# Kernel optimization log

Hardware: AMD Instinct MI355X
Metric: run time of the kernel (lower is better)

Reference implementation:

```python
import jax, jax.numpy as jnp
import numpy as np

B, T, C, H = 2, 2048, 1024, 16


def setup_inputs() -> dict:
    key = jax.random.key(0)
    ks = jax.random.split(key, 9)
    s = 1.0 / np.sqrt(C)
    return {
        "query": jax.random.normal(ks[0], (B, T, C), dtype=jnp.float32),
        "Wq": jax.random.normal(ks[1], (C, C), dtype=jnp.float32) * s,
        "bq": jnp.zeros((C,), dtype=jnp.float32),
        "Wk": jax.random.normal(ks[2], (C, C), dtype=jnp.float32) * s,
        "bk": jnp.zeros((C,), dtype=jnp.float32),
        "Wv": jax.random.normal(ks[3], (C, C), dtype=jnp.float32) * s,
        "bv": jnp.zeros((C,), dtype=jnp.float32),
        "Wp": jax.random.normal(ks[4], (C, C), dtype=jnp.float32) * s,
        "bp": jnp.zeros((C,), dtype=jnp.float32),
        "n_head": H,
    }


def reference(query, Wq, bq, Wk, bk, Wv, bv, Wp, bp, n_head):
    b, t, c = query.shape
    d = c // n_head
    # QKV projections -> [b, h, t, d]
    q = (query @ Wq + bq).reshape(b, t, n_head, d).transpose(0, 2, 1, 3)
    k = (query @ Wk + bk).reshape(b, t, n_head, d).transpose(0, 2, 1, 3)
    v = (query @ Wv + bv).reshape(b, t, n_head, d).transpose(0, 2, 1, 3)
    scale = 1.0 / jnp.sqrt(jnp.asarray(d, dtype=query.dtype))
    att = jnp.einsum('bhtd,bhsd->bhts', q, k) * scale  # [b,h,t,t]
    causal = jnp.tril(jnp.ones((t, t), dtype=bool))
    att = jnp.where(causal[None, None, :, :], att, -jnp.inf)
    att = jax.nn.softmax(att, axis=-1)
    y = jnp.einsum('bhts,bhsd->bhtd', att, v)  # [b,h,t,d]
    y = y.transpose(0, 2, 1, 3).reshape(b, t, c)
    return y @ Wp + bp
```

## Files before the change

### kernel.cpp

```cpp
#include <hip/hip_runtime.h>
#include <math.h>

#define B_ 2
#define T_ 2048
#define C_ 1024
#define H_ 16
#define D_ 64
#define M_ (B_*T_)

typedef __bf16 bf16x8 __attribute__((ext_vector_type(8)));
typedef __bf16 bf16x4 __attribute__((ext_vector_type(4)));
typedef float  f32x4  __attribute__((ext_vector_type(4)));
typedef float  f32x16 __attribute__((ext_vector_type(16)));

__device__ __forceinline__ unsigned short f2bf(float f) {
    unsigned int u = __float_as_uint(f);
    u += 0x7FFFu + ((u >> 16) & 1u);
    return (unsigned short)(u >> 16);
}

__device__ __forceinline__ bf16x8 pack4(unsigned a, unsigned b,
                                        unsigned c, unsigned d) {
    union { unsigned u[4]; bf16x8 v; } t;
    t.u[0] = a; t.u[1] = b; t.u[2] = c; t.u[3] = d;
    return t.v;
}

__device__ __forceinline__ void gload16(const void* g, void* l) {
    __builtin_amdgcn_global_load_lds(
        (const __attribute__((address_space(1))) void*)g,
        (__attribute__((address_space(3))) void*)l, 16, 0, 0);
}

__global__ __launch_bounds__(256) void prep_kernel(
    const float* __restrict__ X, unsigned short* __restrict__ Xb,
    const float* __restrict__ W0, const float* __restrict__ W1,
    const float* __restrict__ W2, const float* __restrict__ W3,
    unsigned short* __restrict__ T0, unsigned short* __restrict__ T1,
    unsigned short* __restrict__ T2, unsigned short* __restrict__ T3)
{
    const int tid = threadIdx.x;
    if (blockIdx.x < 2048) {
        const size_t i = ((size_t)blockIdx.x * 256 + tid) * 8;
        const float4 a = *(const float4*)&X[i];
        const float4 b = *(const float4*)&X[i + 4];
        ushort4 s0, s1;
        s0.x = f2bf(a.x); s0.y = f2bf(a.y); s0.z = f2bf(a.z); s0.w = f2bf(a.w);
        s1.x = f2bf(b.x); s1.y = f2bf(b.y); s1.z = f2bf(b.z); s1.w = f2bf(b.w);
        *(ushort4*)&Xb[i]     = s0;
        *(ushort4*)&Xb[i + 4] = s1;
        return;
    }
    const int bz = blockIdx.x - 2048;
    const int z = bz >> 10, rem = bz & 1023;
    const float* W; unsigned short* Wt;
    switch (z) {
        case 0: W = W0; Wt = T0; break;
        case 1: W = W1; Wt = T1; break;
        case 2: W = W2; Wt = T2; break;
        default: W = W3; Wt = T3; break;
    }
    __shared__ unsigned short tile[32][33];
    const int k0 = (rem >> 5) * 32, n0 = (rem & 31) * 32;
    {
        const int r = tid >> 3, c = (tid & 7) * 4;
        const float4 v = *(const float4*)&W[(size_t)(k0 + r)*C_ + n0 + c];
        tile[c+0][r] = f2bf(v.x);
        tile[c+1][r] = f2bf(v.y);
        tile[c+2][r] = f2bf(v.z);
        tile[c+3][r] = f2bf(v.w);
    }
    __syncthreads();
    {
        const int r = tid >> 3, c = (tid & 7) * 4;
        ushort4 s;
        s.x = tile[r][c+0]; s.y = tile[r][c+1]; s.z = tile[r][c+2]; s.w = tile[r][c+3];
        *(ushort4*)&Wt[(size_t)(n0 + r)*C_ + k0 + c] = s;
    }
}

__global__ __launch_bounds__(256) void gemm_proj_kernel(
    const unsigned short* __restrict__ A, const unsigned short* __restrict__ Bt,
    const float* __restrict__ bias, float* __restrict__ out)
{
    __shared__ __align__(16) unsigned short Als[2][64 * 32];
    __shared__ __align__(16) unsigned short Bls[2][128 * 32];

    const int tid  = threadIdx.x;
    const int lane = tid & 63;
    const int wave = tid >> 6;
    const int wm = wave >> 1, wn = wave & 1;
    const int l15 = lane & 15, quad = lane >> 4;
    const int m0 = blockIdx.y * 64, n0 = blockIdx.x * 128;
    const int srow = lane >> 2;
    const int scol = (lane & 3) * 8;

    const f32x4 zero4 = {0.f, 0.f, 0.f, 0.f};
    f32x4 acc[2][4];
    #pragma unroll
    for (int i = 0; i < 2; ++i)
        #pragma unroll
        for (int j = 0; j < 4; ++j) acc[i][j] = zero4;

    for (int k0 = 0; k0 < C_; k0 += 64) {
        __syncthreads();
        #pragma unroll
        for (int h = 0; h < 2; ++h) {
            gload16(&A[(size_t)(m0 + wave*16 + srow)*C_ + k0 + h*32 + scol],
                    &Als[h][(wave*16)*32]);
            #pragma unroll
            for (int u = 0; u < 2; ++u) {
                const int r = wave*32 + u*16 + srow;
                gload16(&Bt[(size_t)(n0 + r)*C_ + k0 + h*32 + scol],
                        &Bls[h][(wave*32 + u*16)*32]);
            }
        }
        __syncthreads();

        #pragma unroll
        for (int h = 0; h < 2; ++h) {
            bf16x8 af[2], bfr[4];
            #pragma unroll
            for (int i = 0; i < 2; ++i)
                af[i] = *(const bf16x8*)&Als[h][(wm*32 + i*16 + l15)*32 + quad*8];
            #pragma unroll
            for (int j = 0; j < 4; ++j)
                bfr[j] = *(const bf16x8*)&Bls[h][(wn*64 + j*16 + l15)*32 + quad*8];

            #pragma unroll
            for (int i = 0; i < 2; ++i)
                #pragma unroll
                for (int j = 0; j < 4; ++j)
                    acc[i][j] = __builtin_amdgcn_mfma_f32_16x16x32_bf16(
                        af[i], bfr[j], acc[i][j], 0, 0, 0);
        }
    }

    #pragma unroll
    for (int j = 0; j < 4; ++j) {
        const int n = n0 + wn*64 + j*16 + l15;
        const float bv = bias[n];
        #pragma unroll
        for (int i = 0; i < 2; ++i)
            #pragma unroll
            for (int r = 0; r < 4; ++r) {
                const int m = m0 + wm*32 + i*16 + quad*4 + r;
                out[(size_t)m*C_ + n] = acc[i][j][r] + bv;
            }
    }
}

__global__ __launch_bounds__(512, 2) void gemm256_qkv_kernel(
    const unsigned short* __restrict__ A, const unsigned short* __restrict__ Bt,
    const float* __restrict__ b0, const float* __restrict__ b1,
    const float* __restrict__ b2,
    unsigned short* __restrict__ outq, unsigned short* __restrict__ outk,
    unsigned short* __restrict__ outv)
{
    __shared__ __align__(16) unsigned short lds[4 * 16384];

    const int tid  = threadIdx.x;
    const int lane = tid & 63;
    const int wave = tid >> 6;
    const int l15  = lane & 15, quad = lane >> 4;
    const int wm   = wave >> 2, wn = wave & 3;
    const int bid  = blockIdx.y * 12 + blockIdx.x;
    const int swz  = (bid & 7) * 24 + (bid >> 3);
    const int m0   = (swz / 12) * 256, n0 = (swz % 12) * 256;

    const int lrow = lane >> 2;
    const int csw  = ((lane & 3) ^ ((lane >> 3) & 3)) * 8;
    const int sw8  = (quad ^ ((l15 >> 1) & 3)) * 8;

#define STAGE_H(tt, h) do {                                                    \
        const int bi_ = ((tt) & 3) << 14;                                      \
        const int k0_ = (tt) << 5;                                             \
        const int ra_ = m0 + wave*32 + (h)*16 + lrow;                          \
        const int rb_ = n0 + wave*32 + (h)*16 + lrow;                          \
        gload16(&A [(size_t)ra_*C_ + k0_ + csw],                               \
                &lds[bi_ + wave*1024 + (h)*512]);                              \
        gload16(&Bt[(size_t)rb_*C_ + k0_ + csw],                               \
                &lds[bi_ + 8192 + wave*1024 + (h)*512]);                       \
    } while (0)

    const f32x4 zero4 = {0.f, 0.f, 0.f, 0.f};
    f32x4 acc[8][4];
    #pragma unroll
    for (int i = 0; i < 8; ++i)
        #pragma unroll
        for (int j = 0; j < 4; ++j) acc[i][j] = zero4;

    STAGE_H(0,0); STAGE_H(0,1);
    STAGE_H(1,0); STAGE_H(1,1);
    STAGE_H(2,0); STAGE_H(2,1);

    for (int t = 0; t < 32; ++t) {
        const int bi = (t & 3) << 14;
        __builtin_amdgcn_s_barrier();
        __builtin_amdgcn_sched_barrier(0);
        if (t <= 29) {
            asm volatile("s_waitcnt vmcnt(8)" ::: "memory");
        } else if (t == 30) {
            asm volatile("s_waitcnt vmcnt(4)" ::: "memory");
        } else {
            asm volatile("s_waitcnt vmcnt(0)" ::: "memory");
        }
        __builtin_amdgcn_s_barrier();
        __builtin_amdgcn_sched_barrier(0);

        const unsigned short* Ab = &lds[bi];
        const unsigned short* Bb = &lds[bi + 8192];

        bf16x8 bfr[4], af[4];
        #pragma unroll
        for (int j = 0; j < 4; ++j)
            bfr[j] = *(const bf16x8*)&Bb[(wn*64 + j*16 + l15)*32 + sw8];
        #pragma unroll
        for (int i = 0; i < 4; ++i)
            af[i] = *(const bf16x8*)&Ab[(wm*128 + i*16 + l15)*32 + sw8];

        if (t < 29) STAGE_H(t + 3, 0);

        __builtin_amdgcn_s_setprio(1);
        #pragma unroll
        for (int i = 0; i < 4; ++i)
            #pragma unroll
            for (int j = 0; j < 4; ++j)
                acc[i][j] = __builtin_amdgcn_mfma_f32_16x16x32_bf16(
                    af[i], bfr[j], acc[i][j], 0, 0, 0);
        __builtin_amdgcn_s_setprio(0);

        __builtin_amdgcn_s_barrier();
        __builtin_amdgcn_sched_barrier(0);

        #pragma unroll
        for (int i = 0; i < 4; ++i)
            af[i] = *(const bf16x8*)&Ab[(wm*128 + 64 + i*16 + l15)*32 + sw8];

        if (t < 29) STAGE_H(t + 3, 1);

        __builtin_amdgcn_s_setprio(1);
        #pragma unroll
        for (int i = 0; i < 4; ++i)
            #pragma unroll
            for (int j = 0; j < 4; ++j)
                acc[4+i][j] = __builtin_amdgcn_mfma_f32_16x16x32_bf16(
                    af[i], bfr[j], acc[4+i][j], 0, 0, 0);
        __builtin_amdgcn_s_setprio(0);
    }
#undef STAGE_H

    __syncthreads();

    unsigned short* Ep = &lds[wave * 8192];
    const int which = n0 >> 10;
    const int c0 = (n0 & 1023) + wn * 64;
    const int h  = c0 >> 6;
    const int bb = m0 >> 11;
    const int t0 = (m0 & (T_ - 1)) + wm * 128;
    const int bh = bb * H_ + h;
    const float* bp = (which == 0) ? b0 : (which == 1 ? b1 : b2);
    const float qscale = (which == 0) ? 0.18033688f : 1.0f;

    if (which < 2) {
        __bf16* Eb = (__bf16*)Ep;
        #pragma unroll
        for (int j = 0; j < 4; ++j) {
            const int cl = j*16 + l15;
            const float bias = bp[c0 + cl];
            #pragma unroll
            for (int i = 0; i < 8; ++i)
                #pragma unroll
                for (int r = 0; r < 4; ++r)
                    Eb[(i*16 + quad*4 + r)*64 + cl] =
                        (__bf16)((acc[i][j][r] + bias) * qscale);
        }
        unsigned short* op = (which == 0) ? outq : outk;
        const int row8 = lane >> 3, chunk = lane & 7;
        #pragma unroll
        for (int u = 0; u < 16; ++u) {
            const int row = u*8 + row8;
            const uint4 v = *(const uint4*)&Ep[row*64 + chunk*8];
            *(uint4*)&op[((size_t)bh*T_ + t0 + row)*D_ + chunk*8] = v;
        }
    } else {
        #pragma unroll
        for (int j = 0; j < 4; ++j) {
            const int cl = j*16 + l15;
            const float bias = bp[c0 + cl];
            const int xo = (cl & 7) * 8;
            #pragma unroll
            for (int i = 0; i < 8; ++i) {
                bf16x4 pk = {(__bf16)(acc[i][j][0] + bias),
                             (__bf16)(acc[i][j][1] + bias),
                             (__bf16)(acc[i][j][2] + bias),
                             (__bf16)(acc[i][j][3] + bias)};
                *(bf16x4*)&Ep[cl*128 + ((i*16 + quad*4) ^ xo)] = pk;
            }
        }
        const int d4 = lane >> 4, chunk = lane & 15;
        #pragma unroll
        for (int u = 0; u < 16; ++u) {
            const int d = u*4 + d4;
            const uint4 v = *(const uint4*)&Ep[d*128 + ((chunk*8) ^ ((d & 7)*8))];
            *(uint4*)&outv[((size_t)bh*D_ + d)*T_ + t0 + chunk*8] = v;
        }
    }
}

__global__ __launch_bounds__(256) void flash_mfma_kernel(
    const unsigned short* __restrict__ Qs, const unsigned short* __restrict__ Ks,
    const unsigned short* __restrict__ Vts, unsigned short* __restrict__ Y,
    float* __restrict__ parts, float* __restrict__ lbase)
{
    __shared__ __align__(16) unsigned short Kls[64 * 64];
    __shared__ __align__(16) unsigned short Vls[64 * 64];
    __shared__ float lsums[4][32];

    const int tid  = threadIdx.x;
    const int lane = tid & 63, wave = tid >> 6;
    const int krl  = lane & 31, hi = lane >> 5;
    const int srow8 = lane >> 3;
    const int schk8 = ((lane & 7) ^ srow8) * 8;
    const int job  = blockIdx.x >> 5;
    const int bh   = blockIdx.x & 31;
    const bool isA = (job < 8);
    const int a    = isA ? job : job - 8;

    int qts[2], slos[2], shis[2], slots[2], nseg;
    if (isA) {
        qts[0] = a;      slos[0] = 0;        shis[0] = 2*a + 2;  slots[0] = -1;
        qts[1] = 15 - a; slos[1] = 0;        shis[1] = 15 - 2*a; slots[1] = 0;
        nseg = 2;
    } else {
        qts[0] = 15 - a; slos[0] = 15 - 2*a; shis[0] = 32 - 2*a; slots[0] = 1;
        nseg = 1;
    }

    const int b_ = bh >> 4, h_ = bh & (H_ - 1);

#define FSTAGE(itv) do {                                                       \
        const int s0_ = (itv) * 64;                                            \
        const int cu0_ = 2*wave, cu1_ = 2*wave + 1;                            \
        const int r0_ = cu0_*8 + srow8, r1_ = cu1_*8 + srow8;                  \
        gload16(&Ks [((size_t)bh*T_ + s0_ + r0_)*D_ + schk8],                  \
                (char*)Kls + cu0_*1024);                                       \
        gload16(&Vts[((size_t)bh*D_ + r0_)*T_ + s0_ + schk8],                  \
                (char*)Vls + cu0_*1024);                                       \
        gload16(&Ks [((size_t)bh*T_ + s0_ + r1_)*D_ + schk8],                  \
                (char*)Kls + cu1_*1024);                                       \
        gload16(&Vts[((size_t)bh*D_ + r1_)*T_ + s0_ + schk8],                  \
                (char*)Vls + cu1_*1024);                                       \
    } while (0)

    for (int sg = 0; sg < nseg; ++sg) {
        const int qt  = qts[sg];
        const int qw0 = qt * 128 + wave * 32;
        const int qrow = qw0 + krl;

        bf16x8 qf[4];
        #pragma unroll
        for (int ds = 0; ds < 4; ++ds)
            qf[ds] = *(const bf16x8*)&Qs[((size_t)bh*T_ + qrow)*D_ + ds*16 + hi*8];

        f32x16 o[2];
        #pragma unroll
        for (int dt = 0; dt < 2; ++dt)
            #pragma unroll
            for (int r = 0; r < 16; ++r) o[dt][r] = 0.f;
        float lsum = 0.f;

        for (int it = slos[sg]; it < shis[sg]; ++it) {
            const int s0 = it * 64;
            __syncthreads();
            FSTAGE(it);
            __syncthreads();

            if (s0 > qw0 + 31) continue;

            f32x16 st[2];
            #pragma unroll
            for (int kt = 0; kt < 2; ++kt)
                #pragma unroll
                for (int r = 0; r < 16; ++r) st[kt][r] = 0.f;
            #pragma unroll
            for (int kt = 0; kt < 2; ++kt) {
                #pragma unroll
                for (int ds = 0; ds < 4; ++ds) {
                    const int row = kt*32 + krl;
                    bf16x8 kf = *(const bf16x8*)
                        &Kls[row*64 + (((ds*2 + hi) ^ (krl & 7)) << 3)];
                    st[kt] = __builtin_amdgcn_mfma_f32_32x32x16_bf16(
                        kf, qf[ds], st[kt], 0, 0, 0);
                }
            }

            const bool diag = (s0 + 63 > qw0);
            #pragma unroll
            for (int kt = 0; kt < 2; ++kt) {
                const int kb = s0 + kt*32 + 4*hi;
                #pragma unroll
                for (int reg = 0; reg < 16; ++reg) {
                    const int crow = (reg & 3) + 8*(reg >> 2);
                    float e = __builtin_amdgcn_exp2f(st[kt][reg]);
                    if (diag && (kb + crow > qrow)) e = 0.f;
                    st[kt][reg] = e;
                    lsum += e;
                }
            }

            bf16x8 pa[4];
            #pragma unroll
            for (int kt = 0; kt < 2; ++kt) {
                #pragma unroll
                for (int hh = 0; hh < 2; ++hh) {
                    const int rb = hh * 8;
                    unsigned c0, c1, c2, c3;
                    asm("v_cvt_pk_bf16_f32 %0, %1, %2"
                        : "=v"(c0) : "v"(st[kt][rb+0]), "v"(st[kt][rb+1]));
                    asm("v_cvt_pk_bf16_f32 %0, %1, %2"
                        : "=v"(c1) : "v"(st[kt][rb+2]), "v"(st[kt][rb+3]));
                    asm("v_cvt_pk_bf16_f32 %0, %1, %2"
                        : "=v"(c2) : "v"(st[kt][rb+4]), "v"(st[kt][rb+5]));
                    asm("v_cvt_pk_bf16_f32 %0, %1, %2"
                        : "=v"(c3) : "v"(st[kt][rb+6]), "v"(st[kt][rb+7]));
                    asm("v_permlane32_swap_b32 %0, %1" : "+v"(c0), "+v"(c2));
                    asm("v_permlane32_swap_b32 %0, %1" : "+v"(c1), "+v"(c3));
                    pa[kt*2 + hh] = pack4(c0, c1, c2, c3);
                }
            }

            #pragma unroll
            for (int dt = 0; dt < 2; ++dt) {
                #pragma unroll
                for (int ks = 0; ks < 4; ++ks) {
                    const int rowd = dt*32 + krl;
                    bf16x8 vb = *(const bf16x8*)
                        &Vls[rowd*64 + (((ks*2 + hi) ^ (krl & 7)) << 3)];
                    o[dt] = __builtin_amdgcn_mfma_f32_32x32x16_bf16(
                        pa[ks], vb, o[dt], 0, 0, 0);
                }
            }
        }

        lsum += __shfl_xor(lsum, 32, 64);
        if (lane < 32) lsums[wave][krl] = lsum;

        if (slots[sg] < 0) {
            #pragma unroll
            for (int reg = 0; reg < 16; ++reg) {
                const int q = (reg & 3) + 8*(reg >> 2) + 4*hi;
                const float inv = 1.0f / lsums[wave][q];
                const size_t yb = ((size_t)(b_*T_ + qw0 + q))*C_ + h_*D_;
                *(__bf16*)&Y[yb + krl]      = (__bf16)(o[0][reg] * inv);
                *(__bf16*)&Y[yb + 32 + krl] = (__bf16)(o[1][reg] * inv);
            }
        } else {
            const int gpi = bh*16 + a*2 + slots[sg];
            float* Op = parts + (size_t)gpi*8192;
            float* Lp = lbase + gpi*128;
            if (lane < 32) Lp[wave*32 + lane] = lsum;
            #pragma unroll
            for (int reg = 0; reg < 16; ++reg) {
                const int tl = wave*32 + (reg & 3) + 8*(reg >> 2) + 4*hi;
                Op[(size_t)tl*64 + krl]      = o[0][reg];
                Op[(size_t)tl*64 + 32 + krl] = o[1][reg];
            }
        }
    }
#undef FSTAGE
}

__global__ __launch_bounds__(256) void merge_kernel(
    const float* __restrict__ parts, const float* __restrict__ lbase,
    unsigned short* __restrict__ Y)
{
    const int pair = blockIdx.x;
    const int bh = pair >> 3, p = pair & 7;
    const int qt = 15 - p;
    const int g0 = bh*16 + p*2;
    const float* O0 = parts + (size_t)g0*8192;
    const float* O1 = O0 + 8192;
    const float* L0 = lbase + g0*128;
    const float* L1 = L0 + 128;

    const int tid = threadIdx.x;
    const int r = tid >> 1, c0 = (tid & 1) * 32;
    const float inv = 1.0f / (L0[r] + L1[r]);
    const int b = bh >> 4, h = bh & (H_ - 1);
    const int t = qt*128 + r;
    #pragma unroll
    for (int k = 0; k < 8; ++k) {
        const f32x4 a  = *(const f32x4*)&O0[(size_t)r*64 + c0 + k*4];
        const f32x4 bb = *(const f32x4*)&O1[(size_t)r*64 + c0 + k*4];
        bf16x4 pk = {(__bf16)((a[0]+bb[0])*inv), (__bf16)((a[1]+bb[1])*inv),
                     (__bf16)((a[2]+bb[2])*inv), (__bf16)((a[3]+bb[3])*inv)};
        *(bf16x4*)&Y[((size_t)(b*T_ + t))*C_ + h*D_ + c0 + k*4] = pk;
    }
}

extern "C" void kernel_launch(void* const* d_in, const int* in_sizes, int n_in,
                              void* d_out, int out_size, void* d_ws, size_t ws_size,
                              hipStream_t stream) {
    const float* query = (const float*)d_in[0];
    const float* Wq = (const float*)d_in[1];
    const float* bq = (const float*)d_in[2];
    const float* Wk = (const float*)d_in[3];
    const float* bk = (const float*)d_in[4];
    const float* Wv = (const float*)d_in[5];
    const float* bv = (const float*)d_in[6];
    const float* Wp = (const float*)d_in[7];
    const float* bp = (const float*)d_in[8];
    float* out = (float*)d_out;

    char* ws = (char*)d_ws;
    unsigned short* qbf   = (unsigned short*)(ws);
    unsigned short* kbf   = (unsigned short*)(ws + 8388608);
    unsigned short* vtbf  = (unsigned short*)(ws + 16777216);
    unsigned short* WtP   = (unsigned short*)(ws + 25165824);
    unsigned short* WtQKV = (unsigned short*)(ws + 27262976);
    unsigned short* yb    = (unsigned short*)(ws + 33554432);
    unsigned short* qx    = (unsigned short*)(ws + 41943040);
    float* lbase = (float*)(ws + 27262976);
    float* parts = out;

    prep_kernel<<<6144, 256, 0, stream>>>(
        query, qx, Wq, Wk, Wv, Wp,
        WtQKV, WtQKV + (size_t)C_*C_, WtQKV + 2*(size_t)C_*C_, WtP);

    gemm256_qkv_kernel<<<dim3(12, 16), 512, 0, stream>>>(
        qx, WtQKV, bq, bk, bv, qbf, kbf, vtbf);

    flash_mfma_kernel<<<512, 256, 0, stream>>>(qbf, kbf, vtbf, yb, parts, lbase);
    merge_kernel<<<256, 256, 0, stream>>>(parts, lbase, yb);

    gemm_proj_kernel<<<dim3(C_/128, M_/64), 256, 0, stream>>>(
        yb, WtP, bp, out);
}
```

Measured before the change: 186.7 us.

## Pipeline output-projection GEMM with 4-stage async LDS ring and swizzled layout

Replaces the single-buffered load-then-compute loop in the output projection GEMM with a 4-slot LDS ring buffer that keeps three K-tiles of global-to-LDS loads in flight, using explicit vmcnt waits and barriers. It also XOR-swizzles the LDS column layout to reduce bank conflicts on fragment reads, and raises wave priority around the MFMA block. The aim is to hide global load latency behind compute. In exchange it uses more LDS, which may lower occupancy, and it relies on hand-tuned waitcnt values being correct.

New measurement: 187.6 us. About the same (+0.5%).

```diff
diff --git a/kernel.cpp b/kernel.cpp
--- a/kernel.cpp
+++ b/kernel.cpp
@@ -83,8 +83,7 @@
     const unsigned short* __restrict__ A, const unsigned short* __restrict__ Bt,
     const float* __restrict__ bias, float* __restrict__ out)
 {
-    __shared__ __align__(16) unsigned short Als[2][64 * 32];
-    __shared__ __align__(16) unsigned short Bls[2][128 * 32];
+    __shared__ __align__(16) unsigned short lds[4 * 6144];
 
     const int tid  = threadIdx.x;
     const int lane = tid & 63;
@@ -92,8 +91,21 @@
     const int wm = wave >> 1, wn = wave & 1;
     const int l15 = lane & 15, quad = lane >> 4;
     const int m0 = blockIdx.y * 64, n0 = blockIdx.x * 128;
-    const int srow = lane >> 2;
-    const int scol = (lane & 3) * 8;
+
+    const int lrow = lane >> 2;
+    const int csw  = ((lane & 3) ^ ((lane >> 3) & 3)) * 8;
+    const int sw8  = (quad ^ ((l15 >> 1) & 3)) * 8;
+
+#define PSTAGE(tt) do {                                                        \
+        const int bi_ = ((tt) & 3) * 6144;                                     \
+        const int k0_ = (tt) << 5;                                             \
+        gload16(&A [(size_t)(m0 + wave*16 + lrow)*C_ + k0_ + csw],             \
+                &lds[bi_ + wave*512]);                                         \
+        gload16(&Bt[(size_t)(n0 + wave*32 + lrow)*C_ + k0_ + csw],             \
+                &lds[bi_ + 2048 + wave*1024]);                                 \
+        gload16(&Bt[(size_t)(n0 + wave*32 + 16 + lrow)*C_ + k0_ + csw],        \
+                &lds[bi_ + 2048 + wave*1024 + 512]);                           \
+    } while (0)
 
     const f32x4 zero4 = {0.f, 0.f, 0.f, 0.f};
     f32x4 acc[2][4];
@@ -102,39 +114,45 @@
         #pragma unroll
         for (int j = 0; j < 4; ++j) acc[i][j] = zero4;
 
-    for (int k0 = 0; k0 < C_; k0 += 64) {
-        __syncthreads();
-        #pragma unroll
-        for (int h = 0; h < 2; ++h) {
-            gload16(&A[(size_t)(m0 + wave*16 + srow)*C_ + k0 + h*32 + scol],
-                    &Als[h][(wave*16)*32]);
-            #pragma unroll
-            for (int u = 0; u < 2; ++u) {
-                const int r = wave*32 + u*16 + srow;
-                gload16(&Bt[(size_t)(n0 + r)*C_ + k0 + h*32 + scol],
-                        &Bls[h][(wave*32 + u*16)*32]);
-            }
-        }
-        __syncthreads();
-
-        #pragma unroll
-        for (int h = 0; h < 2; ++h) {
-            bf16x8 af[2], bfr[4];
-            #pragma unroll
-            for (int i = 0; i < 2; ++i)
-                af[i] = *(const bf16x8*)&Als[h][(wm*32 + i*16 + l15)*32 + quad*8];
+    PSTAGE(0); PSTAGE(1); PSTAGE(2);
+
+    for (int t = 0; t < 32; ++t) {
+        const int bi = (t & 3) * 6144;
+        __builtin_amdgcn_s_barrier();
+        __builtin_amdgcn_sched_barrier(0);
+        if (t <= 29) {
+            asm volatile("s_waitcnt vmcnt(6)" ::: "memory");
+        } else if (t == 30) {
+            asm volatile("s_waitcnt vmcnt(3)" ::: "memory");
+        } else {
+            asm volatile("s_waitcnt vmcnt(0)" ::: "memory");
+        }
+        __builtin_amdgcn_s_barrier();
+        __builtin_amdgcn_sched_barrier(0);
+
+        const unsigned short* Ab = &lds[bi];
+        const unsigned short* Bb = &lds[bi + 2048];
+
+        bf16x8 af[2], bfr[4];
+        #pragma unroll
+        for (int i = 0; i < 2; ++i)
+            af[i] = *(const bf16x8*)&Ab[(wm*32 + i*16 + l15)*32 + sw8];
+        #pragma unroll
+        for (int j = 0; j < 4; ++j)
+            bfr[j] = *(const bf16x8*)&Bb[(wn*64 + j*16 + l15)*32 + sw8];
+
+        if (t < 29) PSTAGE(t + 3);
+
+        __builtin_amdgcn_s_setprio(1);
+        #pragma unroll
+        for (int i = 0; i < 2; ++i)
             #pragma unroll
             for (int j = 0; j < 4; ++j)
-                bfr[j] = *(const bf16x8*)&Bls[h][(wn*64 + j*16 + l15)*32 + quad*8];
-
-            #pragma unroll
-            for (int i = 0; i < 2; ++i)
-                #pragma unroll
-                for (int j = 0; j < 4; ++j)
-                    acc[i][j] = __builtin_amdgcn_mfma_f32_16x16x32_bf16(
-                        af[i], bfr[j], acc[i][j], 0, 0, 0);
-        }
-    }
+                acc[i][j] = __builtin_amdgcn_mfma_f32_16x16x32_bf16(
+                    af[i], bfr[j], acc[i][j], 0, 0, 0);
+        __builtin_amdgcn_s_setprio(0);
+    }
+#undef PSTAGE
 
     #pragma unroll
     for (int j = 0; j < 4; ++j) {
```
